# Kernel tuning notes

Measured on AMD Instinct MI355X. Metric: run time of the kernel, lower is better.

The kernel has to match this reference:

```python
import jax, jax.numpy as jnp
import numpy as np

GRIDS = ((16, 16, 16), (32, 16, 8), (8, 32, 16))  # prod == 4096 == N_p for each scale
PAIRS = ((0, 1), (0, 2), (1, 2))
KVOL = 27.0  # 3x3x3 kernel, count_include_pad=True -> always divide by 27


def _avg_pool3(x):
    # x: [B, C, d, h, w]; avg_pool3d kernel 3, stride 1, pad 1 (shape preserving)
    s = jax.lax.reduce_window(
        x, 0.0, jax.lax.add,
        window_dimensions=(1, 1, 3, 3, 3),
        window_strides=(1, 1, 1, 1, 1),
        padding=((0, 0), (0, 0), (1, 1), (1, 1), (1, 1)))
    return s / KVOL


def _window(feat, grid):
    # feat: [B, N, D] -> raw reshape into [B, D, d, h, w] (layout-mixing, faithful to torch .reshape)
    B, N, D = feat.shape
    x = feat.reshape(B, -1, *grid)
    p = _avg_pool3(x)
    return p.reshape(B, p.shape[1], -1).transpose(0, 2, 1)  # [B, N, D]


def setup_inputs() -> dict:
    key = jax.random.key(0)
    ks = jax.random.split(key, 8)
    B, N, D = 8, 4096, 512
    e0 = jax.random.normal(ks[0], (B, N, D), jnp.float32)
    e1 = jax.random.normal(ks[1], (B, N, D), jnp.float32)
    e2 = jax.random.normal(ks[2], (B, N, D), jnp.float32)
    W1 = jax.random.normal(ks[3], (3, 2 * D, D), jnp.float32) * 0.02
    b1 = jnp.zeros((3, D), jnp.float32)
    W2 = jax.random.normal(ks[4], (3, D, 1), jnp.float32) * 0.02
    b2 = jnp.zeros((3, 1), jnp.float32)
    gamma = jnp.ones((D,), jnp.float32)
    beta = jnp.zeros((D,), jnp.float32)
    Wf = jax.random.normal(ks[5], (D, D), jnp.float32) * 0.02
    bf = jnp.zeros((D,), jnp.float32)
    return dict(e0=e0, e1=e1, e2=e2, W1=W1, b1=b1, W2=W2, b2=b2,
                gamma=gamma, beta=beta, Wf=Wf, bf=bf)


def reference(e0, e1, e2, W1, b1, W2, b2, gamma, beta, Wf, bf):
    embeds = (e0, e1, e2)
    windows = [_window(embeds[s], GRIDS[s]) for s in range(3)]  # each [B, N, D]
    matched = []
    for k, (i, j) in enumerate(PAIRS):
        def mlp(c):
            h = jax.nn.relu(jnp.einsum('bne,ed->bnd', c, W1[k]) + b1[k])
            return jnp.einsum('bnd,do->bno', h, W2[k]) + b2[k]  # [B, N, 1]
        cij = jnp.concatenate([windows[i], windows[j]], axis=-1)  # [B, N, 2D]
        cji = jnp.concatenate([windows[j], windows[i]], axis=-1)
        aij = jax.nn.softmax(mlp(cij), axis=1)
        aji = jax.nn.softmax(mlp(cji), axis=1)
        matched.append(jnp.sum(aij * embeds[j], axis=1, keepdims=True))  # [B, 1, D]
        matched.append(jnp.sum(aji * embeds[i], axis=1, keepdims=True))
    fused = jnp.concatenate(list(embeds) + matched, axis=1).mean(axis=1)  # [B, D]
    mu = fused.mean(axis=-1, keepdims=True)
    var = fused.var(axis=-1, keepdims=True)
    ln = (fused - mu) / jnp.sqrt(var + 1e-5) * gamma + beta
    return ln @ Wf + bf  # [B, D]
```

## Files before the change

kernel.cpp:

```cpp
#include <hip/hip_runtime.h>
#include <hip/hip_bf16.h>

typedef unsigned short u16;
typedef __bf16 bf16x8 __attribute__((ext_vector_type(8)));
typedef float f32x4 __attribute__((ext_vector_type(4)));


static __device__ __forceinline__ u16 f2bf(float f) {
  unsigned u = __builtin_bit_cast(unsigned, f);
  unsigned r = (u + 0x7FFFu + ((u >> 16) & 1u)) >> 16;
  return (u16)r;
}

__global__ __launch_bounds__(512) void k_poolpack(const float* __restrict__ e0,
                                                  const float* __restrict__ e1,
                                                  const float* __restrict__ e2,
                                                  u16* __restrict__ packA,
                                                  int b0, int nb) {
  __shared__ __align__(16) float v[4096];
  __shared__ __align__(16) float t1[4096];
  __shared__ __align__(16) u16 outp[16384];
  int bx = blockIdx.x;
  int cg4 = bx & 127;
  int q = bx >> 7;
  int scale = q / nb;
  int lb = q - scale * nb;
  int b = b0 + lb;
  const float* eptr = scale == 0 ? e0 : (scale == 1 ? e1 : e2);
  const int LW = (scale == 0) ? 4 : (scale == 1 ? 3 : 4);
  const int LHW = (scale == 0) ? 8 : (scale == 1 ? 7 : 9);
  const int w = 1 << LW, hw = 1 << LHW;
  const int h = hw >> LW;
  const int dep = 4096 >> LHW;
  int t = threadIdx.x;
  int c0 = cg4 * 4;
  for (int ci = 0; ci < 4; ++ci) {
    const float* src = eptr + (size_t)b * 2097152 + (size_t)(c0 + ci) * 4096;
    ((float4*)v)[t] = ((const float4*)src)[t];
    ((float4*)v)[t + 512] = ((const float4*)src)[t + 512];
    __syncthreads();
    for (int j = 0; j < 8; ++j) {
      int s = t + j * 512;
      int x = s & (w - 1);
      float sum = v[s];
      if (x > 0) sum += v[s - 1];
      if (x < w - 1) sum += v[s + 1];
      t1[s] = sum;
    }
    __syncthreads();
    for (int j = 0; j < 8; ++j) {
      int s = t + j * 512;
      int y = (s >> LW) & (h - 1);
      float sum = t1[s];
      if (y > 0) sum += t1[s - w];
      if (y < h - 1) sum += t1[s + w];
      v[s] = sum;
    }
    __syncthreads();
    for (int j = 0; j < 8; ++j) {
      int s = t + j * 512;
      int z = s >> LHW;
      float sum = v[s];
      if (z > 0) sum += v[s - hw];
      if (z < dep - 1) sum += v[s + hw];
      outp[s * 4 + ci] = f2bf(sum * (1.0f / 27.0f));
    }
    __syncthreads();
  }
  int cb = c0 >> 5;
  int hi = (c0 >> 3) & 3;
  int eh = (c0 >> 2) & 1;
  size_t blk = (size_t)(lb * 3 + scale) * 2097152;
  for (int k2 = 0; k2 < 8; ++k2) {
    int s = t + k2 * 512;
    int2 val = *(const int2*)&outp[s * 4];
    size_t dst = blk + ((size_t)(s >> 4) * 16 + cb) * 512 +
                 (size_t)(hi * 16 + (s & 15)) * 8 + eh * 4;
    *(int2*)(packA + dst) = val;
  }
}

__global__ __launch_bounds__(64) void k_packW(const float* __restrict__ W1,
                                              u16* __restrict__ W1p) {
  int u = blockIdx.x;
  int kb = u & 31;
  int nb_ = (u >> 5) & 31;
  int kp = u >> 10;
  int l = threadIdx.x;
  int m = l & 15, hi = l >> 4;
  u16 tmp[8];
  for (int e = 0; e < 8; ++e) {
    int kg = kb * 32 + hi * 8 + e;
    tmp[e] = f2bf(W1[((size_t)kp * 1024 + kg) * 512 + nb_ * 16 + m]);
  }
  *(int4*)(W1p + ((size_t)u * 64 + l) * 8) = *(int4*)tmp;
}

__global__ __launch_bounds__(256, 3) void k_gemm(const u16* __restrict__ packA,
                                                 const u16* __restrict__ W1p,
                                                 const float* __restrict__ b1,
                                                 const float* __restrict__ W2,
                                                 float* __restrict__ logits,
                                                 int b0, int nb) {
  __shared__ __align__(16) u16 abuf[2][4096];
  __shared__ __align__(16) u16 bbuf[2][4096];
  __shared__ float red[2][128];
  int per = gridDim.x >> 3;
  int logical = (blockIdx.x & 7) * per + (blockIdx.x >> 3);
  int nt = logical & 3;
  int mt = (logical >> 2) & 31;
  int rest = logical >> 7;
  int lb = rest % nb;
  int dir = rest / nb;
  int b = b0 + lb;
  int kp = dir >> 1, sw = dir & 1;
  const int PI[3] = {0, 0, 1}, PJ[3] = {1, 2, 2};
  int pi = PI[kp], pj = PJ[kp];
  int first = sw ? pj : pi;
  int second = sw ? pi : pj;
  int t = threadIdx.x;
  int w = t >> 6;
  int l = t & 63;
  int wr = w & 1, wc = w >> 1;
  const u16* Abase1 = packA + (size_t)(lb * 3 + first) * 2097152;
  const u16* Abase2 = packA + (size_t)(lb * 3 + second) * 2097152;

  f32x4 acc[4][4];
  for (int a = 0; a < 4; ++a)
    for (int n = 0; n < 4; ++n) acc[a][n] = (f32x4){0.f, 0.f, 0.f, 0.f};

#define STAGE(BUFI, T)                                                            \
  do {                                                                            \
    const u16* P_ = ((T) < 16) ? Abase1 : Abase2;                                 \
    int cb_ = (T) & 15;                                                           \
    for (int r_ = 0; r_ < 2; ++r_) {                                              \
      int u_ = r_ * 4 + w;                                                        \
      const u16* g_ = P_ + ((size_t)((mt * 8 + u_) * 16 + cb_)) * 512 +           \
                      (size_t)l * 8;                                              \
      __builtin_amdgcn_global_load_lds(                                           \
          (const __attribute__((address_space(1))) void*)g_,                      \
          (__attribute__((address_space(3))) void*)&abuf[BUFI][u_ * 512],         \
          16, 0, 0);                                                              \
    }                                                                             \
    for (int r_ = 0; r_ < 2; ++r_) {                                              \
      int u_ = r_ * 4 + w;                                                        \
      const u16* g_ = W1p + ((size_t)((kp * 32 + nt * 8 + u_) * 32 + (T))) * 512 +\
                      (size_t)l * 8;                                              \
      __builtin_amdgcn_global_load_lds(                                           \
          (const __attribute__((address_space(1))) void*)g_,                      \
          (__attribute__((address_space(3))) void*)&bbuf[BUFI][u_ * 512],         \
          16, 0, 0);                                                              \
    }                                                                             \
  } while (0)

#define COMPUTE(BUFI)                                                             \
  do {                                                                            \
    bf16x8 af[4], bfr[4];                                                         \
    _Pragma("unroll")                                                             \
    for (int mi = 0; mi < 4; ++mi)                                                \
      af[mi] = *(const bf16x8*)&abuf[BUFI][(wr * 4 + mi) * 512 + l * 8];          \
    _Pragma("unroll")                                                             \
    for (int ni = 0; ni < 4; ++ni)                                                \
      bfr[ni] = *(const bf16x8*)&bbuf[BUFI][(wc * 4 + ni) * 512 + l * 8];         \
    _Pragma("unroll")                                                             \
    for (int mi = 0; mi < 4; ++mi)                                                \
      _Pragma("unroll")                                                           \
      for (int ni = 0; ni < 4; ++ni)                                              \
        acc[mi][ni] = __builtin_amdgcn_mfma_f32_16x16x32_bf16(                    \
            af[mi], bfr[ni], acc[mi][ni], 0, 0, 0);                               \
  } while (0)

  STAGE(0, 0);
  for (int tt = 0; tt < 31; ++tt) {
    STAGE((tt + 1) & 1, tt + 1);
    asm volatile("s_waitcnt vmcnt(4)" ::: "memory");
    __builtin_amdgcn_sched_barrier(0);
    __builtin_amdgcn_s_barrier();
    COMPUTE(tt & 1);
    __builtin_amdgcn_s_barrier();
  }
  asm volatile("s_waitcnt vmcnt(0)" ::: "memory");
  __builtin_amdgcn_sched_barrier(0);
  __builtin_amdgcn_s_barrier();
  COMPUTE(1);
#undef STAGE
#undef COMPUTE

  int m = l & 15, hi = l >> 4;
  float w2v[4], b1v[4];
  for (int ni = 0; ni < 4; ++ni) {
    int n = nt * 128 + wc * 64 + ni * 16 + m;
    w2v[ni] = W2[kp * 512 + n];
    b1v[ni] = b1[kp * 512 + n];
  }
  for (int mi = 0; mi < 4; ++mi)
    for (int r = 0; r < 4; ++r) {
      float s = 0.f;
      for (int ni = 0; ni < 4; ++ni) {
        float h = acc[mi][ni][r] + b1v[ni];
        s += fmaxf(h, 0.f) * w2v[ni];
      }
      float vv = s;
      vv += __shfl_xor(vv, 1);
      vv += __shfl_xor(vv, 2);
      vv += __shfl_xor(vv, 4);
      vv += __shfl_xor(vv, 8);
      if (m == 0) red[wc][wr * 64 + mi * 16 + hi * 4 + r] = vv;
    }
  __syncthreads();
  if (t < 128) {
    float s = red[0][t] + red[1][t];
    atomicAdd(&logits[((size_t)dir * 8 + b) * 4096 + mt * 128 + t], s);
  }
}

__global__ __launch_bounds__(256) void k_softmax(float* __restrict__ logits) {
  __shared__ __align__(16) float buf[4096];
  __shared__ float wred[4];
  int row = blockIdx.x;
  float* p = logits + (size_t)row * 4096;
  int t = threadIdx.x;
  float lmax = -1e30f;
  for (int j = 0; j < 4; ++j) {
    float4 v = ((const float4*)p)[t + j * 256];
    v.x = fmaxf(fminf(v.x, 1e4f), -1e4f);
    v.y = fmaxf(fminf(v.y, 1e4f), -1e4f);
    v.z = fmaxf(fminf(v.z, 1e4f), -1e4f);
    v.w = fmaxf(fminf(v.w, 1e4f), -1e4f);
    ((float4*)buf)[t + j * 256] = v;
    lmax = fmaxf(lmax, fmaxf(fmaxf(v.x, v.y), fmaxf(v.z, v.w)));
  }
  for (int off = 1; off < 64; off <<= 1) lmax = fmaxf(lmax, __shfl_xor(lmax, off));
  if ((t & 63) == 0) wred[t >> 6] = lmax;
  __syncthreads();
  float gmax = fmaxf(fmaxf(wred[0], wred[1]), fmaxf(wred[2], wred[3]));
  __syncthreads();
  float lsum = 0.f;
  for (int j = 0; j < 16; ++j) {
    int s = t + j * 256;
    float ex = expf(buf[s] - gmax);
    buf[s] = ex;
    lsum += ex;
  }
  for (int off = 1; off < 64; off <<= 1) lsum += __shfl_xor(lsum, off);
  if ((t & 63) == 0) wred[t >> 6] = lsum;
  __syncthreads();
  float inv = 1.f / (wred[0] + wred[1] + wred[2] + wred[3]);
  for (int j = 0; j < 4; ++j) {
    int i4 = t + j * 256;
    float4 v = ((const float4*)buf)[i4];
    v.x *= inv; v.y *= inv; v.z *= inv; v.w *= inv;
    ((float4*)p)[i4] = v;
  }
}

__global__ void k_zero(float* __restrict__ p, int n) {
  int i = blockIdx.x * 256 + threadIdx.x;
  if (i < n) p[i] = 0.f;
}

__global__ __launch_bounds__(256) void k_matched(const float* __restrict__ e0,
                                                 const float* __restrict__ e1,
                                                 const float* __restrict__ e2,
                                                 const float* __restrict__ wts,
                                                 float* __restrict__ fused) {
  __shared__ float lw[384];
  int bx = blockIdx.x;
  int nc = bx & 63;
  int b = bx >> 6;
  int n0 = nc * 64;
  int t = threadIdx.x;
  for (int idx = t; idx < 384; idx += 256) {
    int dir = idx >> 6, nn = idx & 63;
    lw[idx] = wts[((size_t)dir * 8 + b) * 4096 + n0 + nn];
  }
  __syncthreads();
  size_t base = (size_t)b * 2097152 + (size_t)n0 * 512;
  const float2* p0 = (const float2*)(e0 + base) + t;
  const float2* p1 = (const float2*)(e1 + base) + t;
  const float2* p2 = (const float2*)(e2 + base) + t;
  float2 tot = {0.f, 0.f};
  float2 m0 = {0, 0}, m1 = {0, 0}, m2 = {0, 0}, m3 = {0, 0}, m4 = {0, 0}, m5 = {0, 0};
  for (int nn = 0; nn < 64; ++nn) {
    float2 v0 = p0[nn * 256];
    float2 v1 = p1[nn * 256];
    float2 v2 = p2[nn * 256];
    tot.x += v0.x + v1.x + v2.x;
    tot.y += v0.y + v1.y + v2.y;
    float w0 = lw[0 * 64 + nn], w1 = lw[1 * 64 + nn], w2 = lw[2 * 64 + nn];
    float w3 = lw[3 * 64 + nn], w4 = lw[4 * 64 + nn], w5 = lw[5 * 64 + nn];
    m0.x += w0 * v1.x; m0.y += w0 * v1.y;
    m1.x += w1 * v0.x; m1.y += w1 * v0.y;
    m2.x += w2 * v2.x; m2.y += w2 * v2.y;
    m3.x += w3 * v0.x; m3.y += w3 * v0.y;
    m4.x += w4 * v2.x; m4.y += w4 * v2.y;
    m5.x += w5 * v1.x; m5.y += w5 * v1.y;
  }
  float rx = tot.x + m0.x + m1.x + m2.x + m3.x + m4.x + m5.x;
  float ry = tot.y + m0.y + m1.y + m2.y + m3.y + m4.y + m5.y;
  atomicAdd(&fused[b * 512 + 2 * t], rx);
  atomicAdd(&fused[b * 512 + 2 * t + 1], ry);
}

__global__ __launch_bounds__(512) void k_final(const float* __restrict__ fused,
                                               const float* __restrict__ gamma,
                                               const float* __restrict__ beta,
                                               const float* __restrict__ Wf,
                                               const float* __restrict__ bfv,
                                               float* __restrict__ out) {
  __shared__ float lnv[512];
  __shared__ float sred[16];
  __shared__ float pred[4][128];
  int bx = blockIdx.x;
  int db = bx & 3, b = bx >> 2;
  int t = threadIdx.x;
  float f = fused[b * 512 + t] * (1.0f / 12294.0f);
  float s1 = f, s2 = f * f;
  for (int off = 1; off < 64; off <<= 1) {
    s1 += __shfl_xor(s1, off);
    s2 += __shfl_xor(s2, off);
  }
  if ((t & 63) == 0) {
    sred[(t >> 6) * 2] = s1;
    sred[(t >> 6) * 2 + 1] = s2;
  }
  __syncthreads();
  float S1 = 0.f, S2 = 0.f;
  for (int ww = 0; ww < 8; ++ww) {
    S1 += sred[ww * 2];
    S2 += sred[ww * 2 + 1];
  }
  float mu = S1 * (1.0f / 512.0f);
  float var = S2 * (1.0f / 512.0f) - mu * mu;
  float rstd = rsqrtf(var + 1e-5f);
  lnv[t] = (f - mu) * rstd * gamma[t] + beta[t];
  __syncthreads();
  int dt = t & 127, eq = t >> 7;
  int d = db * 128 + dt;
  float acc = 0.f;
  for (int e = eq * 128; e < eq * 128 + 128; ++e)
    acc += lnv[e] * Wf[(size_t)e * 512 + d];
  pred[eq][dt] = acc;
  __syncthreads();
  if (t < 128) {
    float r = pred[0][t] + pred[1][t] + pred[2][t] + pred[3][t] + bfv[db * 128 + t];
    out[b * 512 + db * 128 + t] = r;
  }
}

extern "C" void kernel_launch(void* const* d_in, const int* in_sizes, int n_in,
                              void* d_out, int out_size, void* d_ws, size_t ws_size,
                              hipStream_t stream) {
  const float* e0 = (const float*)d_in[0];
  const float* e1 = (const float*)d_in[1];
  const float* e2 = (const float*)d_in[2];
  const float* W1 = (const float*)d_in[3];
  const float* b1 = (const float*)d_in[4];
  const float* W2 = (const float*)d_in[5];
  const float* gamma = (const float*)d_in[7];
  const float* beta = (const float*)d_in[8];
  const float* Wf = (const float*)d_in[9];
  const float* bf = (const float*)d_in[10];

  char* ws = (char*)d_ws;
  float* fused = (float*)ws;
  float* logits = (float*)(ws + 16384);
  u16* W1p = (u16*)(ws + 802816);
  u16* packA = (u16*)(ws + 3948544);
  int nbat = 8;
  while (nbat > 1 && 3948544 + (size_t)nbat * 12582912 > ws_size) nbat >>= 1;

  hipLaunchKernelGGL(k_zero, dim3(784), dim3(256), 0, stream, fused, 200704);
  hipLaunchKernelGGL(k_packW, dim3(3072), dim3(64), 0, stream, W1, W1p);
  for (int b0 = 0; b0 < 8; b0 += nbat) {
    hipLaunchKernelGGL(k_poolpack, dim3(3 * nbat * 128), dim3(512), 0, stream,
                       e0, e1, e2, packA, b0, nbat);
    hipLaunchKernelGGL(k_gemm, dim3(768 * nbat), dim3(256), 0, stream,
                       packA, W1p, b1, W2, logits, b0, nbat);
  }
  hipLaunchKernelGGL(k_softmax, dim3(48), dim3(256), 0, stream, logits);
  hipLaunchKernelGGL(k_matched, dim3(512), dim3(256), 0, stream, e0, e1, e2, logits, fused);
  hipLaunchKernelGGL(k_final, dim3(32), dim3(512), 0, stream, fused, gamma, beta, Wf, bf,
                     (float*)d_out);
}
```

Before: 537.9 us.

## Triple-buffer GEMM K-loop and reorder block mapping for operand reuse

Extends the LDS staging in the W1 GEMM from double to triple buffering, so two tiles are in flight while one is computed, and adjusts the waitcnt thresholds and loop tail to match. Block index decoding is reordered so the six pair/direction variants for the same row tile and batch are scheduled adjacently, improving L2 reuse of the packed activations. Global addresses are precomputed once per thread instead of rebuilt in each stage. The extra LDS buffer raises shared memory per block, which may limit occupancy.

```diff
diff --git a/kernel.cpp b/kernel.cpp
--- a/kernel.cpp
+++ b/kernel.cpp
@@ -102,16 +102,17 @@
                                                  const float* __restrict__ W2,
                                                  float* __restrict__ logits,
                                                  int b0, int nb) {
-  __shared__ __align__(16) u16 abuf[2][4096];
-  __shared__ __align__(16) u16 bbuf[2][4096];
+  __shared__ __align__(16) u16 abuf[3][4096];
+  __shared__ __align__(16) u16 bbuf[3][4096];
   __shared__ float red[2][128];
   int per = gridDim.x >> 3;
   int logical = (blockIdx.x & 7) * per + (blockIdx.x >> 3);
-  int nt = logical & 3;
-  int mt = (logical >> 2) & 31;
-  int rest = logical >> 7;
-  int lb = rest % nb;
-  int dir = rest / nb;
+  int dir = logical % 6;
+  int r1 = logical / 6;
+  int nt = r1 & 3;
+  int r2 = r1 >> 2;
+  int mt = r2 & 31;
+  int lb = r2 >> 5;
   int b = b0 + lb;
   int kp = dir >> 1, sw = dir & 1;
   const int PI[3] = {0, 0, 1}, PJ[3] = {1, 2, 2};
@@ -122,8 +123,17 @@
   int w = t >> 6;
   int l = t & 63;
   int wr = w & 1, wc = w >> 1;
-  const u16* Abase1 = packA + (size_t)(lb * 3 + first) * 2097152;
-  const u16* Abase2 = packA + (size_t)(lb * 3 + second) * 2097152;
+
+  const u16* a1p[2];
+  const u16* a2p[2];
+  const u16* bp[2];
+  for (int r_ = 0; r_ < 2; ++r_) {
+    int u_ = r_ * 4 + w;
+    size_t aoff = ((size_t)(mt * 8 + u_) * 16) * 512 + (size_t)l * 8;
+    a1p[r_] = packA + (size_t)(lb * 3 + first) * 2097152 + aoff;
+    a2p[r_] = packA + (size_t)(lb * 3 + second) * 2097152 + aoff;
+    bp[r_] = W1p + ((size_t)(kp * 32 + nt * 8 + u_) * 32) * 512 + (size_t)l * 8;
+  }
 
   f32x4 acc[4][4];
   for (int a = 0; a < 4; ++a)
@@ -131,12 +141,10 @@
 
 #define STAGE(BUFI, T)                                                            \
   do {                                                                            \
-    const u16* P_ = ((T) < 16) ? Abase1 : Abase2;                                 \
-    int cb_ = (T) & 15;                                                           \
     for (int r_ = 0; r_ < 2; ++r_) {                                              \
       int u_ = r_ * 4 + w;                                                        \
-      const u16* g_ = P_ + ((size_t)((mt * 8 + u_) * 16 + cb_)) * 512 +           \
-                      (size_t)l * 8;                                              \
+      const u16* g_ = (((T) < 16) ? a1p[r_] : a2p[r_]) +                          \
+                      (size_t)((T) & 15) * 512;                                   \
       __builtin_amdgcn_global_load_lds(                                           \
           (const __attribute__((address_space(1))) void*)g_,                      \
           (__attribute__((address_space(3))) void*)&abuf[BUFI][u_ * 512],         \
@@ -144,8 +152,7 @@
     }                                                                             \
     for (int r_ = 0; r_ < 2; ++r_) {                                              \
       int u_ = r_ * 4 + w;                                                        \
-      const u16* g_ = W1p + ((size_t)((kp * 32 + nt * 8 + u_) * 32 + (T))) * 512 +\
-                      (size_t)l * 8;                                              \
+      const u16* g_ = bp[r_] + (size_t)(T) * 512;                                 \
       __builtin_amdgcn_global_load_lds(                                           \
           (const __attribute__((address_space(1))) void*)g_,                      \
           (__attribute__((address_space(3))) void*)&bbuf[BUFI][u_ * 512],         \
@@ -171,14 +178,21 @@
   } while (0)
 
   STAGE(0, 0);
-  for (int tt = 0; tt < 31; ++tt) {
-    STAGE((tt + 1) & 1, tt + 1);
-    asm volatile("s_waitcnt vmcnt(4)" ::: "memory");
+  STAGE(1, 1);
+#pragma unroll 3
+  for (int tt = 0; tt < 30; ++tt) {
+    STAGE((tt + 2) % 3, tt + 2);
+    asm volatile("s_waitcnt vmcnt(8)" ::: "memory");
     __builtin_amdgcn_sched_barrier(0);
     __builtin_amdgcn_s_barrier();
-    COMPUTE(tt & 1);
+    COMPUTE(tt % 3);
     __builtin_amdgcn_s_barrier();
   }
+  asm volatile("s_waitcnt vmcnt(4)" ::: "memory");
+  __builtin_amdgcn_sched_barrier(0);
+  __builtin_amdgcn_s_barrier();
+  COMPUTE(0);
+  __builtin_amdgcn_s_barrier();
   asm volatile("s_waitcnt vmcnt(0)" ::: "memory");
   __builtin_amdgcn_sched_barrier(0);
   __builtin_amdgcn_s_barrier();
```

After: 538.7 us. No clear change (+0.1%).
